# Kernel optimization log

Hardware: AMD Instinct MI355X
Metric: run time of the kernel (lower is better)

## Reference

```python
import jax, jax.numpy as jnp
import numpy as np

B, T, C = 64, 4096, 256
H = 4
HD = C // H  # head_dim = 64
EPS = 1e-5   # torch LayerNorm default


def setup_inputs() -> dict:
    key = jax.random.key(0)
    ks = jax.random.split(key, 8)
    x = jax.random.normal(ks[0], (B, T, C), dtype=jnp.float32)
    # per-head score MLP: Linear(C->HD) + Tanh + Linear(HD->1, no bias)
    W1 = jax.random.normal(ks[1], (H, C, HD), dtype=jnp.float32) * (1.0 / np.sqrt(C))
    b1 = jax.random.normal(ks[2], (H, HD), dtype=jnp.float32) * 0.02
    w2 = jax.random.normal(ks[3], (H, HD), dtype=jnp.float32) * (1.0 / np.sqrt(HD))
    # output projection Linear(H*C -> C), torch layout (out, in)
    Wo = jax.random.normal(ks[4], (C, H * C), dtype=jnp.float32) * (1.0 / np.sqrt(H * C))
    bo = jax.random.normal(ks[5], (C,), dtype=jnp.float32) * 0.02
    gamma = jnp.ones((C,), dtype=jnp.float32)
    beta = jnp.zeros((C,), dtype=jnp.float32)
    return {"x": x, "W1": W1, "b1": b1, "w2": w2, "Wo": Wo, "bo": bo,
            "gamma": gamma, "beta": beta}


def reference(x, W1, b1, w2, Wo, bo, gamma, beta):
    # All heads batched: hidden (B,H,T,HD)
    h = jnp.tanh(jnp.einsum('btc,hcd->bhtd', x, W1) + b1[None, :, None, :])
    scores = jnp.einsum('bhtd,hd->bht', h, w2)            # (B,H,T)
    weights = jax.nn.softmax(scores, axis=-1)             # softmax over T
    contexts = jnp.einsum('bht,btc->bhc', weights, x)     # (B,H,C)
    multi = contexts.reshape(B, H * C)                    # concat over heads
    out = multi @ Wo.T + bo                               # Linear(H*C->C)
    # LayerNorm over last dim (dropout is identity in eval mode)
    mu = jnp.mean(out, axis=-1, keepdims=True)
    var = jnp.mean(jnp.square(out - mu), axis=-1, keepdims=True)
    out = (out - mu) * jax.lax.rsqrt(var + EPS) * gamma + beta
    return out, weights
```

## Files before the change

kernel.cpp:

```cpp
#include <hip/hip_runtime.h>
#include <hip/hip_bf16.h>
#include <math.h>

#define B_ 64
#define T_ 4096
#define C_ 256
#define H_ 4
#define HD_ 64
#define EPS_ 1e-5f

#define TILE_ 64
#define NBLK_ 64

typedef __attribute__((ext_vector_type(4))) float floatx4;
typedef __attribute__((ext_vector_type(8))) short short8;

#if __has_builtin(__builtin_amdgcn_cvt_pk_bf16_f32)
typedef __attribute__((ext_vector_type(2))) __bf16 bf16x2_t;
__device__ __forceinline__ unsigned int pack_bf16x2(float a, float b) {
    bf16x2_t v = __builtin_amdgcn_cvt_pk_bf16_f32(a, b);
    return __builtin_bit_cast(unsigned int, v);
}
#else
__device__ __forceinline__ unsigned int pack_bf16x2(float a, float b) {
    unsigned int ua = __builtin_bit_cast(unsigned int, a);
    unsigned int ub = __builtin_bit_cast(unsigned int, b);
    ua = (ua + 0x7fffu + ((ua >> 16) & 1u)) >> 16;
    ub = (ub + 0x7fffu + ((ub >> 16) & 1u)) >> 16;
    return ua | (ub << 16);
}
#endif

__device__ __forceinline__ float fast_tanh(float v) {
    float t = v * 2.8853900817779268f;
#if __has_builtin(__builtin_amdgcn_exp2f)
    float e2 = __builtin_amdgcn_exp2f(t);
#else
    float e2 = exp2f(t);
#endif
#if __has_builtin(__builtin_amdgcn_rcpf)
    return fmaf(-2.0f, __builtin_amdgcn_rcpf(e2 + 1.0f), 1.0f);
#else
    return 1.0f - 2.0f / (e2 + 1.0f);
#endif
}

__global__ void k0_w1frag(const float* __restrict__ W1, uint4* __restrict__ w1f) {
    int h  = blockIdx.x >> 3;
    int ks = blockIdx.x & 7;
    int nb = threadIdx.x >> 6;
    int l  = threadIdx.x & 63;
    int nl = l & 15, q = l >> 4;
    int d  = nb * 16 + nl;
    const float* src = W1 + ((long)h * C_ + ks * 32 + q * 8) * HD_ + d;
    float v[8];
    #pragma unroll
    for (int j = 0; j < 8; ++j) v[j] = src[j * HD_];
    uint4 ua;
    ua.x = pack_bf16x2(v[0], v[1]); ua.y = pack_bf16x2(v[2], v[3]);
    ua.z = pack_bf16x2(v[4], v[5]); ua.w = pack_bf16x2(v[6], v[7]);
    w1f[((long)blockIdx.x * 4 + nb) * 64 + l] = ua;
}

#define ASTRIDE 264
__global__ __launch_bounds__(256, 4)
void k1_fused(const float* __restrict__ x, const uint4* __restrict__ w1f,
              const float* __restrict__ b1, const float* __restrict__ w2,
              float* __restrict__ rawscore, float* __restrict__ ctxp,
              float* __restrict__ mS) {
    __shared__ __align__(16) unsigned short shA[TILE_ * ASTRIDE];
    __shared__ float sS[4 * TILE_];
    __shared__ __align__(16) float sP4[TILE_ * 4];

    const int tid  = threadIdx.x;
    const int lane = tid & 63;
    const int w    = tid >> 6;
    const int nl   = lane & 15;
    const int q    = lane >> 4;
    const int rowbase = blockIdx.x * TILE_;
    const int b       = blockIdx.x >> 6;
    const int tbase   = (blockIdx.x & 63) * TILE_;

    const int arow = tid >> 2;
    const int acol = (tid & 3) * 8;
    const float* aptr = x + (long)(rowbase + arow) * C_ + acol;
    #pragma unroll
    for (int kc = 0; kc < 8; ++kc) {
        const float4* ap = (const float4*)(aptr + kc * 32);
        float4 f0 = ap[0], f1 = ap[1];
        uint4 ua;
        ua.x = pack_bf16x2(f0.x, f0.y); ua.y = pack_bf16x2(f0.z, f0.w);
        ua.z = pack_bf16x2(f1.x, f1.y); ua.w = pack_bf16x2(f1.z, f1.w);
        *(uint4*)&shA[arow * ASTRIDE + kc * 32 + acol] = ua;
    }

    floatx4 acc[4][4];
    #pragma unroll
    for (int i = 0; i < 4; ++i)
        #pragma unroll
        for (int j = 0; j < 4; ++j)
            acc[i][j] = (floatx4){0.f, 0.f, 0.f, 0.f};

    const uint4* bW = w1f + (long)w * (8 * 4 * 64) + lane;

    uint4 bFa[4], bFb[4];
    #pragma unroll
    for (int nb = 0; nb < 4; ++nb) bFa[nb] = bW[nb * 64];

    __syncthreads();

    #pragma unroll
    for (int kp = 0; kp < 4; ++kp) {
        const int ks0 = 2 * kp, ks1 = 2 * kp + 1;
        #pragma unroll
        for (int nb = 0; nb < 4; ++nb) bFb[nb] = bW[(ks1 * 4 + nb) * 64];
        #pragma unroll
        for (int mb = 0; mb < 4; ++mb) {
            short8 a = *(const short8*)&shA[(mb * 16 + nl) * ASTRIDE + ks0 * 32 + q * 8];
            #pragma unroll
            for (int nb = 0; nb < 4; ++nb)
                acc[mb][nb] = __builtin_amdgcn_mfma_f32_16x16x32_bf16(
                    a, __builtin_bit_cast(short8, bFa[nb]), acc[mb][nb], 0, 0, 0);
        }
        if (kp < 3) {
            #pragma unroll
            for (int nb = 0; nb < 4; ++nb) bFa[nb] = bW[((ks0 + 2) * 4 + nb) * 64];
        }
        #pragma unroll
        for (int mb = 0; mb < 4; ++mb) {
            short8 a = *(const short8*)&shA[(mb * 16 + nl) * ASTRIDE + ks1 * 32 + q * 8];
            #pragma unroll
            for (int nb = 0; nb < 4; ++nb)
                acc[mb][nb] = __builtin_amdgcn_mfma_f32_16x16x32_bf16(
                    a, __builtin_bit_cast(short8, bFb[nb]), acc[mb][nb], 0, 0, 0);
        }
    }

    float b1v[4], w2v[4];
    #pragma unroll
    for (int nb = 0; nb < 4; ++nb) {
        int d = nb * 16 + nl;
        b1v[nb] = b1[w * HD_ + d];
        w2v[nb] = w2[w * HD_ + d];
    }
    #pragma unroll
    for (int mb = 0; mb < 4; ++mb) {
        float p[4];
        #pragma unroll
        for (int r = 0; r < 4; ++r) {
            float s = 0.f;
            #pragma unroll
            for (int nb = 0; nb < 4; ++nb)
                s += fast_tanh(acc[mb][nb][r] + b1v[nb]) * w2v[nb];
            p[r] = s;
        }
        #pragma unroll
        for (int m = 1; m < 16; m <<= 1)
            #pragma unroll
            for (int r = 0; r < 4; ++r)
                p[r] += __shfl_xor(p[r], m, 64);
        if (nl == 0) {
            #pragma unroll
            for (int r = 0; r < 4; ++r)
                sS[w * TILE_ + mb * 16 + q * 4 + r] = p[r];
        }
    }

    {
        float s = sS[w * TILE_ + lane];
        float m = s;
        #pragma unroll
        for (int off = 1; off < 64; off <<= 1)
            m = fmaxf(m, __shfl_xor(m, off, 64));
        float e = __expf(s - m);
        float Ss = e;
        #pragma unroll
        for (int off = 1; off < 64; off <<= 1)
            Ss += __shfl_xor(Ss, off, 64);
        sP4[lane * 4 + w] = e;
        rawscore[((long)(b * H_ + w)) * T_ + tbase + lane] = s;
        if (lane == 0) {
            mS[((long)blockIdx.x * H_ + w) * 2 + 0] = m;
            mS[((long)blockIdx.x * H_ + w) * 2 + 1] = Ss;
        }
    }
    __syncthreads();

    {
        float c0 = 0.f, c1 = 0.f, c2 = 0.f, c3 = 0.f;
        const float* xr = x + (long)rowbase * C_ + tid;
        const float4* pv4 = (const float4*)sP4;
        #pragma unroll 8
        for (int t = 0; t < TILE_; ++t) {
            float xv = xr[(long)t * C_];
            float4 pv = pv4[t];
            c0 += pv.x * xv;
            c1 += pv.y * xv;
            c2 += pv.z * xv;
            c3 += pv.w * xv;
        }
        float* o = ctxp + (long)blockIdx.x * (H_ * C_) + tid;
        o[0]   = c0;
        o[256] = c1;
        o[512] = c2;
        o[768] = c3;
    }
}

__global__ __launch_bounds__(1024)
void k2_combine(const float* __restrict__ ctxp, const float* __restrict__ mS,
                float* __restrict__ gms, float* __restrict__ multi) {
    __shared__ float sm[NBLK_], sSl[NBLK_];
    __shared__ float red[4][256];
    int bh = blockIdx.x;
    int b = bh >> 2, h = bh & 3;
    int tid = threadIdx.x;
    int c  = tid & 255;
    int js = tid >> 8;
    if (tid < NBLK_) {
        long blk = (long)b * NBLK_ + tid;
        sm[tid]  = mS[(blk * H_ + h) * 2 + 0];
        sSl[tid] = mS[(blk * H_ + h) * 2 + 1];
    }
    __syncthreads();
    float m = -INFINITY;
    #pragma unroll 8
    for (int j = 0; j < NBLK_; ++j) m = fmaxf(m, sm[j]);
    float S = 0.f;
    #pragma unroll 8
    for (int j = 0; j < NBLK_; ++j) S += sSl[j] * __expf(sm[j] - m);
    float invS = 1.0f / S;
    if (tid == 0) { gms[bh * 2 + 0] = m; gms[bh * 2 + 1] = invS; }

    float acc = 0.f;
    #pragma unroll
    for (int jj = 0; jj < NBLK_ / 4; ++jj) {
        int j = js * (NBLK_ / 4) + jj;
        acc += ctxp[((long)(b * NBLK_ + j) * H_ + h) * C_ + c] * __expf(sm[j] - m);
    }
    red[js][c] = acc;
    __syncthreads();
    if (js == 0)
        multi[(long)b * (H_ * C_) + h * C_ + c] =
            (red[0][c] + red[1][c] + red[2][c] + red[3][c]) * invS;
}

__global__ void k3_weights(const float* __restrict__ gms, float* __restrict__ weights) {
    int bh = blockIdx.x >> 1, half = blockIdx.x & 1;
    float m = gms[bh * 2 + 0], invS = gms[bh * 2 + 1];
    float4* wr = (float4*)(weights + (long)bh * T_ + half * 2048);
    int tid = threadIdx.x;
    #pragma unroll
    for (int i = 0; i < 2; ++i) {
        float4 v = wr[tid + i * 256];
        v.x = __expf(v.x - m) * invS;
        v.y = __expf(v.y - m) * invS;
        v.z = __expf(v.z - m) * invS;
        v.w = __expf(v.w - m) * invS;
        wr[tid + i * 256] = v;
    }
}

__global__ __launch_bounds__(256)
void k4a_proj(const float* __restrict__ multiG, const float* __restrict__ Wo,
              const float* __restrict__ bo, float* __restrict__ outraw) {
    __shared__ __align__(16) float multi[1024];
    int b = blockIdx.x >> 4, cs = blockIdx.x & 15;
    int tid = threadIdx.x, w = tid >> 6, l = tid & 63;
    ((float4*)multi)[tid] = ((const float4*)(multiG + (long)b * 1024))[tid];
    __syncthreads();
    float a[4];
    #pragma unroll
    for (int cc = 0; cc < 4; ++cc) {
        int c = cs * 16 + w * 4 + cc;
        const float4* wrow = (const float4*)(Wo + (long)c * 1024);
        const float4* mv = (const float4*)multi;
        float s = 0.f;
        #pragma unroll
        for (int k = 0; k < 4; ++k) {
            float4 wv = wrow[k * 64 + l];
            float4 m4 = mv[k * 64 + l];
            s += wv.x * m4.x + wv.y * m4.y + wv.z * m4.z + wv.w * m4.w;
        }
        a[cc] = s;
    }
    #pragma unroll
    for (int off = 1; off < 64; off <<= 1)
        #pragma unroll
        for (int cc = 0; cc < 4; ++cc)
            a[cc] += __shfl_xor(a[cc], off, 64);
    if (l == 0) {
        #pragma unroll
        for (int cc = 0; cc < 4; ++cc) {
            int c = cs * 16 + w * 4 + cc;
            outraw[(long)b * C_ + c] = a[cc] + bo[c];
        }
    }
}

__global__ void k4b_ln(const float* __restrict__ outraw, const float* __restrict__ gamma,
                       const float* __restrict__ beta, float* __restrict__ out) {
    __shared__ float red[256];
    int b = blockIdx.x, tid = threadIdx.x;
    float acc = outraw[(long)b * C_ + tid];
    red[tid] = acc; __syncthreads();
    for (int st = 128; st > 0; st >>= 1) {
        if (tid < st) red[tid] += red[tid + st];
        __syncthreads();
    }
    float mu = red[0] * (1.0f / 256.0f); __syncthreads();
    float dv = acc - mu;
    red[tid] = dv * dv; __syncthreads();
    for (int st = 128; st > 0; st >>= 1) {
        if (tid < st) red[tid] += red[tid + st];
        __syncthreads();
    }
    float var = red[0] * (1.0f / 256.0f);
    out[(long)b * C_ + tid] = dv * rsqrtf(var + EPS_) * gamma[tid] + beta[tid];
}

extern "C" void kernel_launch(void* const* d_in, const int* in_sizes, int n_in,
                              void* d_out, int out_size, void* d_ws, size_t ws_size,
                              hipStream_t stream) {
    const float* x     = (const float*)d_in[0];
    const float* W1    = (const float*)d_in[1];
    const float* b1    = (const float*)d_in[2];
    const float* w2    = (const float*)d_in[3];
    const float* Wo    = (const float*)d_in[4];
    const float* bo    = (const float*)d_in[5];
    const float* gamma = (const float*)d_in[6];
    const float* beta  = (const float*)d_in[7];

    float* out     = (float*)d_out;
    float* weights = out + B_ * C_;

    const long NB = (long)B_ * NBLK_;
    float* ctxp   = (float*)d_ws;
    float* mS     = ctxp + NB * (H_ * C_);
    float* multi  = mS + NB * H_ * 2;
    uint4* w1f    = (uint4*)(multi + B_ * H_ * C_);
    float* gms    = (float*)w1f + 32768;
    float* outraw = gms + 512;

    k0_w1frag <<<32, 256, 0, stream>>>(W1, w1f);
    k1_fused  <<<NB, 256, 0, stream>>>(x, w1f, b1, w2, weights, ctxp, mS);
    k2_combine<<<256, 1024, 0, stream>>>(ctxp, mS, gms, multi);
    k3_weights<<<512, 256, 0, stream>>>(gms, weights);
    k4a_proj  <<<1024, 256, 0, stream>>>(multi, Wo, bo, outraw);
    k4b_ln    <<<64, 256, 0, stream>>>(outraw, gamma, beta, out);
}
```

Baseline: 423.5 us.

## Make k1 persistent over four tiles with prefetch of the next x tile

k1_fused now launches 1024 blocks, and each block walks four consecutive 64-row tiles instead of one tile per block. While the scoring and softmax of the current tile run, the block loads the next x tile from global memory, converts it to bf16 and writes it into shared memory. The shared-memory write is split into two halves around a barrier so it does not overwrite data still being read. This is meant to hide global load latency and cut per-block launch overhead, at the cost of higher register pressure, fewer blocks in flight, and an extra barrier per tile.

```diff
diff --git a/kernel.cpp b/kernel.cpp
--- a/kernel.cpp
+++ b/kernel.cpp
@@ -11,6 +11,8 @@
 
 #define TILE_ 64
 #define NBLK_ 64
+#define NT_ 4
+#define GRID1_ 1024
 
 typedef __attribute__((ext_vector_type(4))) float floatx4;
 typedef __attribute__((ext_vector_type(8))) short short8;
@@ -77,64 +79,10 @@
     const int w    = tid >> 6;
     const int nl   = lane & 15;
     const int q    = lane >> 4;
-    const int rowbase = blockIdx.x * TILE_;
-    const int b       = blockIdx.x >> 6;
-    const int tbase   = (blockIdx.x & 63) * TILE_;
-
     const int arow = tid >> 2;
     const int acol = (tid & 3) * 8;
-    const float* aptr = x + (long)(rowbase + arow) * C_ + acol;
-    #pragma unroll
-    for (int kc = 0; kc < 8; ++kc) {
-        const float4* ap = (const float4*)(aptr + kc * 32);
-        float4 f0 = ap[0], f1 = ap[1];
-        uint4 ua;
-        ua.x = pack_bf16x2(f0.x, f0.y); ua.y = pack_bf16x2(f0.z, f0.w);
-        ua.z = pack_bf16x2(f1.x, f1.y); ua.w = pack_bf16x2(f1.z, f1.w);
-        *(uint4*)&shA[arow * ASTRIDE + kc * 32 + acol] = ua;
-    }
-
-    floatx4 acc[4][4];
-    #pragma unroll
-    for (int i = 0; i < 4; ++i)
-        #pragma unroll
-        for (int j = 0; j < 4; ++j)
-            acc[i][j] = (floatx4){0.f, 0.f, 0.f, 0.f};
 
     const uint4* bW = w1f + (long)w * (8 * 4 * 64) + lane;
-
-    uint4 bFa[4], bFb[4];
-    #pragma unroll
-    for (int nb = 0; nb < 4; ++nb) bFa[nb] = bW[nb * 64];
-
-    __syncthreads();
-
-    #pragma unroll
-    for (int kp = 0; kp < 4; ++kp) {
-        const int ks0 = 2 * kp, ks1 = 2 * kp + 1;
-        #pragma unroll
-        for (int nb = 0; nb < 4; ++nb) bFb[nb] = bW[(ks1 * 4 + nb) * 64];
-        #pragma unroll
-        for (int mb = 0; mb < 4; ++mb) {
-            short8 a = *(const short8*)&shA[(mb * 16 + nl) * ASTRIDE + ks0 * 32 + q * 8];
-            #pragma unroll
-            for (int nb = 0; nb < 4; ++nb)
-                acc[mb][nb] = __builtin_amdgcn_mfma_f32_16x16x32_bf16(
-                    a, __builtin_bit_cast(short8, bFa[nb]), acc[mb][nb], 0, 0, 0);
-        }
-        if (kp < 3) {
-            #pragma unroll
-            for (int nb = 0; nb < 4; ++nb) bFa[nb] = bW[((ks0 + 2) * 4 + nb) * 64];
-        }
-        #pragma unroll
-        for (int mb = 0; mb < 4; ++mb) {
-            short8 a = *(const short8*)&shA[(mb * 16 + nl) * ASTRIDE + ks1 * 32 + q * 8];
-            #pragma unroll
-            for (int nb = 0; nb < 4; ++nb)
-                acc[mb][nb] = __builtin_amdgcn_mfma_f32_16x16x32_bf16(
-                    a, __builtin_bit_cast(short8, bFb[nb]), acc[mb][nb], 0, 0, 0);
-        }
-    }
 
     float b1v[4], w2v[4];
     #pragma unroll
@@ -143,67 +91,180 @@
         b1v[nb] = b1[w * HD_ + d];
         w2v[nb] = w2[w * HD_ + d];
     }
-    #pragma unroll
-    for (int mb = 0; mb < 4; ++mb) {
-        float p[4];
-        #pragma unroll
-        for (int r = 0; r < 4; ++r) {
-            float s = 0.f;
-            #pragma unroll
-            for (int nb = 0; nb < 4; ++nb)
-                s += fast_tanh(acc[mb][nb][r] + b1v[nb]) * w2v[nb];
-            p[r] = s;
-        }
-        #pragma unroll
-        for (int m = 1; m < 16; m <<= 1)
-            #pragma unroll
-            for (int r = 0; r < 4; ++r)
-                p[r] += __shfl_xor(p[r], m, 64);
-        if (nl == 0) {
-            #pragma unroll
-            for (int r = 0; r < 4; ++r)
-                sS[w * TILE_ + mb * 16 + q * 4 + r] = p[r];
-        }
-    }
 
     {
-        float s = sS[w * TILE_ + lane];
-        float m = s;
-        #pragma unroll
-        for (int off = 1; off < 64; off <<= 1)
-            m = fmaxf(m, __shfl_xor(m, off, 64));
-        float e = __expf(s - m);
-        float Ss = e;
-        #pragma unroll
-        for (int off = 1; off < 64; off <<= 1)
-            Ss += __shfl_xor(Ss, off, 64);
-        sP4[lane * 4 + w] = e;
-        rawscore[((long)(b * H_ + w)) * T_ + tbase + lane] = s;
-        if (lane == 0) {
-            mS[((long)blockIdx.x * H_ + w) * 2 + 0] = m;
-            mS[((long)blockIdx.x * H_ + w) * 2 + 1] = Ss;
-        }
-    }
+        const int rb0 = (blockIdx.x * NT_) * TILE_;
+        const float* aptr = x + (long)(rb0 + arow) * C_ + acol;
+        #pragma unroll
+        for (int kc = 0; kc < 8; ++kc) {
+            const float4* ap = (const float4*)(aptr + kc * 32);
+            float4 f0 = ap[0], f1 = ap[1];
+            uint4 ua;
+            ua.x = pack_bf16x2(f0.x, f0.y); ua.y = pack_bf16x2(f0.z, f0.w);
+            ua.z = pack_bf16x2(f1.x, f1.y); ua.w = pack_bf16x2(f1.z, f1.w);
+            *(uint4*)&shA[arow * ASTRIDE + kc * 32 + acol] = ua;
+        }
+    }
+    uint4 bFa[4], bFb[4];
+    #pragma unroll
+    for (int nb = 0; nb < 4; ++nb) bFa[nb] = bW[nb * 64];
     __syncthreads();
 
-    {
-        float c0 = 0.f, c1 = 0.f, c2 = 0.f, c3 = 0.f;
-        const float* xr = x + (long)rowbase * C_ + tid;
-        const float4* pv4 = (const float4*)sP4;
-        #pragma unroll 8
-        for (int t = 0; t < TILE_; ++t) {
-            float xv = xr[(long)t * C_];
-            float4 pv = pv4[t];
-            c0 += pv.x * xv;
-            c1 += pv.y * xv;
-            c2 += pv.z * xv;
-            c3 += pv.w * xv;
-        }
-        float* o = ctxp + (long)blockIdx.x * (H_ * C_) + tid;
-        o[0]   = c0;
-        o[256] = c1;
-        o[512] = c2;
-        o[768] = c3;
+    #pragma unroll 1
+    for (int it = 0; it < NT_; ++it) {
+        const int tile    = blockIdx.x * NT_ + it;
+        const int rowbase = tile * TILE_;
+        const int b       = tile >> 6;
+        const int tbase   = (tile & 63) * TILE_;
+        const bool more   = (it + 1 < NT_);
+        const float* aN   = x + (long)(rowbase + TILE_ + arow) * C_ + acol;
+
+        floatx4 acc[4][4];
+        #pragma unroll
+        for (int i = 0; i < 4; ++i)
+            #pragma unroll
+            for (int j = 0; j < 4; ++j)
+                acc[i][j] = (floatx4){0.f, 0.f, 0.f, 0.f};
+        #pragma unroll
+        for (int kp = 0; kp < 4; ++kp) {
+            const int ks0 = 2 * kp, ks1 = 2 * kp + 1;
+            #pragma unroll
+            for (int nb = 0; nb < 4; ++nb) bFb[nb] = bW[(ks1 * 4 + nb) * 64];
+            #pragma unroll
+            for (int mb = 0; mb < 4; ++mb) {
+                short8 a = *(const short8*)&shA[(mb * 16 + nl) * ASTRIDE + ks0 * 32 + q * 8];
+                #pragma unroll
+                for (int nb = 0; nb < 4; ++nb)
+                    acc[mb][nb] = __builtin_amdgcn_mfma_f32_16x16x32_bf16(
+                        a, __builtin_bit_cast(short8, bFa[nb]), acc[mb][nb], 0, 0, 0);
+            }
+            if (kp < 3) {
+                #pragma unroll
+                for (int nb = 0; nb < 4; ++nb) bFa[nb] = bW[((ks0 + 2) * 4 + nb) * 64];
+            }
+            #pragma unroll
+            for (int mb = 0; mb < 4; ++mb) {
+                short8 a = *(const short8*)&shA[(mb * 16 + nl) * ASTRIDE + ks1 * 32 + q * 8];
+                #pragma unroll
+                for (int nb = 0; nb < 4; ++nb)
+                    acc[mb][nb] = __builtin_amdgcn_mfma_f32_16x16x32_bf16(
+                        a, __builtin_bit_cast(short8, bFb[nb]), acc[mb][nb], 0, 0, 0);
+            }
+        }
+        #pragma unroll
+        for (int nb = 0; nb < 4; ++nb) bFa[nb] = bW[nb * 64];
+
+        float4 f0h[4], f1h[4];
+        if (more) {
+            #pragma unroll
+            for (int kc = 0; kc < 4; ++kc) {
+                const float4* ap = (const float4*)(aN + kc * 32);
+                f0h[kc] = ap[0]; f1h[kc] = ap[1];
+            }
+        }
+
+        #pragma unroll
+        for (int mb = 0; mb < 4; ++mb) {
+            float p[4];
+            #pragma unroll
+            for (int r = 0; r < 4; ++r) {
+                float s = 0.f;
+                #pragma unroll
+                for (int nb = 0; nb < 4; ++nb)
+                    s += fast_tanh(acc[mb][nb][r] + b1v[nb]) * w2v[nb];
+                p[r] = s;
+            }
+            #pragma unroll
+            for (int m = 1; m < 16; m <<= 1)
+                #pragma unroll
+                for (int r = 0; r < 4; ++r)
+                    p[r] += __shfl_xor(p[r], m, 64);
+            if (nl == 0) {
+                #pragma unroll
+                for (int r = 0; r < 4; ++r)
+                    sS[w * TILE_ + mb * 16 + q * 4 + r] = p[r];
+            }
+        }
+
+        uint4 stA[4];
+        if (more) {
+            #pragma unroll
+            for (int kc = 0; kc < 4; ++kc) {
+                stA[kc].x = pack_bf16x2(f0h[kc].x, f0h[kc].y);
+                stA[kc].y = pack_bf16x2(f0h[kc].z, f0h[kc].w);
+                stA[kc].z = pack_bf16x2(f1h[kc].x, f1h[kc].y);
+                stA[kc].w = pack_bf16x2(f1h[kc].z, f1h[kc].w);
+            }
+        }
+
+        {
+            float s = sS[w * TILE_ + lane];
+            float m = s;
+            #pragma unroll
+            for (int off = 1; off < 64; off <<= 1)
+                m = fmaxf(m, __shfl_xor(m, off, 64));
+            float e = __expf(s - m);
+            float Ss = e;
+            #pragma unroll
+            for (int off = 1; off < 64; off <<= 1)
+                Ss += __shfl_xor(Ss, off, 64);
+            sP4[lane * 4 + w] = e;
+            rawscore[((long)(b * H_ + w)) * T_ + tbase + lane] = s;
+            if (lane == 0) {
+                mS[((long)tile * H_ + w) * 2 + 0] = m;
+                mS[((long)tile * H_ + w) * 2 + 1] = Ss;
+            }
+        }
+
+        float4 f0g[4], f1g[4];
+        if (more) {
+            #pragma unroll
+            for (int kc = 0; kc < 4; ++kc) {
+                const float4* ap = (const float4*)(aN + (kc + 4) * 32);
+                f0g[kc] = ap[0]; f1g[kc] = ap[1];
+            }
+        }
+
+        __syncthreads();
+
+        if (more) {
+            #pragma unroll
+            for (int kc = 0; kc < 4; ++kc)
+                *(uint4*)&shA[arow * ASTRIDE + kc * 32 + acol] = stA[kc];
+        }
+
+        {
+            float c0 = 0.f, c1 = 0.f, c2 = 0.f, c3 = 0.f;
+            const float* xr = x + (long)rowbase * C_ + tid;
+            const float4* pv4 = (const float4*)sP4;
+            #pragma unroll 8
+            for (int t = 0; t < TILE_; ++t) {
+                float xv = xr[(long)t * C_];
+                float4 pv = pv4[t];
+                c0 += pv.x * xv;
+                c1 += pv.y * xv;
+                c2 += pv.z * xv;
+                c3 += pv.w * xv;
+            }
+            float* o = ctxp + (long)tile * (H_ * C_) + tid;
+            o[0]   = c0;
+            o[256] = c1;
+            o[512] = c2;
+            o[768] = c3;
+        }
+
+        if (more) {
+            #pragma unroll
+            for (int kc = 0; kc < 4; ++kc) {
+                uint4 ub;
+                ub.x = pack_bf16x2(f0g[kc].x, f0g[kc].y);
+                ub.y = pack_bf16x2(f0g[kc].z, f0g[kc].w);
+                ub.z = pack_bf16x2(f1g[kc].x, f1g[kc].y);
+                ub.w = pack_bf16x2(f1g[kc].z, f1g[kc].w);
+                *(uint4*)&shA[arow * ASTRIDE + (kc + 4) * 32 + acol] = ub;
+            }
+            __syncthreads();
+        }
     }
 }
 
@@ -343,7 +404,7 @@
     float* outraw = gms + 512;
 
     k0_w1frag <<<32, 256, 0, stream>>>(W1, w1f);
-    k1_fused  <<<NB, 256, 0, stream>>>(x, w1f, b1, w2, weights, ctxp, mS);
+    k1_fused  <<<GRID1_, 256, 0, stream>>>(x, w1f, b1, w2, weights, ctxp, mS);
     k2_combine<<<256, 1024, 0, stream>>>(ctxp, mS, gms, multi);
     k3_weights<<<512, 256, 0, stream>>>(gms, weights);
     k4a_proj  <<<1024, 256, 0, stream>>>(multi, Wo, bo, outraw);
```

New measurement: 734.5 us. +73.4%, slower.

## Fold softmax normalization into combine kernel and fuse projection with LayerNorm

Applied to the files above, without the earlier changes.

The separate weights-normalization kernel is removed: the combine kernel now rescales each (b,h) row of raw scores (1024 threads × float4 = 4096) with the global max and inverse sum it has just computed. The output projection and LayerNorm are merged into one 64-block kernel of 1024 threads that keeps the projected row in shared memory. This cuts two kernel launches and the intermediate buffers for max/sum and the raw projection output. The trade-off is that the fused projection runs on only 64 blocks instead of 1024, so each block streams the full Wo matrix with less parallelism.

```diff
diff --git a/kernel.cpp b/kernel.cpp
--- a/kernel.cpp
+++ b/kernel.cpp
@@ -209,7 +209,7 @@
 
 __global__ __launch_bounds__(1024)
 void k2_combine(const float* __restrict__ ctxp, const float* __restrict__ mS,
-                float* __restrict__ gms, float* __restrict__ multi) {
+                float* __restrict__ weights, float* __restrict__ multi) {
     __shared__ float sm[NBLK_], sSl[NBLK_];
     __shared__ float red[4][256];
     int bh = blockIdx.x;
@@ -230,93 +230,79 @@
     #pragma unroll 8
     for (int j = 0; j < NBLK_; ++j) S += sSl[j] * __expf(sm[j] - m);
     float invS = 1.0f / S;
-    if (tid == 0) { gms[bh * 2 + 0] = m; gms[bh * 2 + 1] = invS; }
-
-    float acc = 0.f;
-    #pragma unroll
-    for (int jj = 0; jj < NBLK_ / 4; ++jj) {
-        int j = js * (NBLK_ / 4) + jj;
-        acc += ctxp[((long)(b * NBLK_ + j) * H_ + h) * C_ + c] * __expf(sm[j] - m);
-    }
-    red[js][c] = acc;
-    __syncthreads();
-    if (js == 0)
-        multi[(long)b * (H_ * C_) + h * C_ + c] =
-            (red[0][c] + red[1][c] + red[2][c] + red[3][c]) * invS;
-}
-
-__global__ void k3_weights(const float* __restrict__ gms, float* __restrict__ weights) {
-    int bh = blockIdx.x >> 1, half = blockIdx.x & 1;
-    float m = gms[bh * 2 + 0], invS = gms[bh * 2 + 1];
-    float4* wr = (float4*)(weights + (long)bh * T_ + half * 2048);
-    int tid = threadIdx.x;
-    #pragma unroll
-    for (int i = 0; i < 2; ++i) {
-        float4 v = wr[tid + i * 256];
+
+    {
+        float4* wr = (float4*)(weights + (long)bh * T_);
+        float4 v = wr[tid];
         v.x = __expf(v.x - m) * invS;
         v.y = __expf(v.y - m) * invS;
         v.z = __expf(v.z - m) * invS;
         v.w = __expf(v.w - m) * invS;
-        wr[tid + i * 256] = v;
-    }
-}
-
-__global__ __launch_bounds__(256)
-void k4a_proj(const float* __restrict__ multiG, const float* __restrict__ Wo,
-              const float* __restrict__ bo, float* __restrict__ outraw) {
-    __shared__ __align__(16) float multi[1024];
-    int b = blockIdx.x >> 4, cs = blockIdx.x & 15;
-    int tid = threadIdx.x, w = tid >> 6, l = tid & 63;
-    ((float4*)multi)[tid] = ((const float4*)(multiG + (long)b * 1024))[tid];
-    __syncthreads();
-    float a[4];
-    #pragma unroll
-    for (int cc = 0; cc < 4; ++cc) {
-        int c = cs * 16 + w * 4 + cc;
+        wr[tid] = v;
+    }
+
+    float acc = 0.f;
+    #pragma unroll
+    for (int jj = 0; jj < NBLK_ / 4; ++jj) {
+        int j = js * (NBLK_ / 4) + jj;
+        acc += ctxp[((long)(b * NBLK_ + j) * H_ + h) * C_ + c] * __expf(sm[j] - m);
+    }
+    red[js][c] = acc;
+    __syncthreads();
+    if (js == 0)
+        multi[(long)b * (H_ * C_) + h * C_ + c] =
+            (red[0][c] + red[1][c] + red[2][c] + red[3][c]) * invS;
+}
+
+__global__ __launch_bounds__(1024)
+void k4_fused(const float* __restrict__ multiG, const float* __restrict__ Wo,
+              const float* __restrict__ bo, const float* __restrict__ gamma,
+              const float* __restrict__ beta, float* __restrict__ out) {
+    __shared__ float sOut[256];
+    __shared__ float red[256];
+    int b = blockIdx.x, tid = threadIdx.x, w = tid >> 6, l = tid & 63;
+
+    float4 mreg[4];
+    const float4* mv = (const float4*)(multiG + (long)b * 1024);
+    #pragma unroll
+    for (int k = 0; k < 4; ++k) mreg[k] = mv[k * 64 + l];
+
+    #pragma unroll
+    for (int cc = 0; cc < 16; ++cc) {
+        int c = w * 16 + cc;
         const float4* wrow = (const float4*)(Wo + (long)c * 1024);
-        const float4* mv = (const float4*)multi;
         float s = 0.f;
         #pragma unroll
         for (int k = 0; k < 4; ++k) {
             float4 wv = wrow[k * 64 + l];
-            float4 m4 = mv[k * 64 + l];
-            s += wv.x * m4.x + wv.y * m4.y + wv.z * m4.z + wv.w * m4.w;
-        }
-        a[cc] = s;
-    }
-    #pragma unroll
-    for (int off = 1; off < 64; off <<= 1)
-        #pragma unroll
-        for (int cc = 0; cc < 4; ++cc)
-            a[cc] += __shfl_xor(a[cc], off, 64);
-    if (l == 0) {
-        #pragma unroll
-        for (int cc = 0; cc < 4; ++cc) {
-            int c = cs * 16 + w * 4 + cc;
-            outraw[(long)b * C_ + c] = a[cc] + bo[c];
-        }
-    }
-}
-
-__global__ void k4b_ln(const float* __restrict__ outraw, const float* __restrict__ gamma,
-                       const float* __restrict__ beta, float* __restrict__ out) {
-    __shared__ float red[256];
-    int b = blockIdx.x, tid = threadIdx.x;
-    float acc = outraw[(long)b * C_ + tid];
-    red[tid] = acc; __syncthreads();
+            s += wv.x * mreg[k].x + wv.y * mreg[k].y + wv.z * mreg[k].z + wv.w * mreg[k].w;
+        }
+        #pragma unroll
+        for (int off = 1; off < 64; off <<= 1)
+            s += __shfl_xor(s, off, 64);
+        if (l == 0) sOut[c] = s + bo[c];
+    }
+    __syncthreads();
+
+    float acc = 0.f;
+    if (tid < 256) { acc = sOut[tid]; red[tid] = acc; }
+    __syncthreads();
     for (int st = 128; st > 0; st >>= 1) {
         if (tid < st) red[tid] += red[tid + st];
         __syncthreads();
     }
-    float mu = red[0] * (1.0f / 256.0f); __syncthreads();
+    float mu = red[0] * (1.0f / 256.0f);
+    __syncthreads();
     float dv = acc - mu;
-    red[tid] = dv * dv; __syncthreads();
+    if (tid < 256) red[tid] = dv * dv;
+    __syncthreads();
     for (int st = 128; st > 0; st >>= 1) {
         if (tid < st) red[tid] += red[tid + st];
         __syncthreads();
     }
     float var = red[0] * (1.0f / 256.0f);
-    out[(long)b * C_ + tid] = dv * rsqrtf(var + EPS_) * gamma[tid] + beta[tid];
+    if (tid < 256)
+        out[(long)b * C_ + tid] = dv * rsqrtf(var + EPS_) * gamma[tid] + beta[tid];
 }
 
 extern "C" void kernel_launch(void* const* d_in, const int* in_sizes, int n_in,
@@ -339,13 +325,9 @@
     float* mS     = ctxp + NB * (H_ * C_);
     float* multi  = mS + NB * H_ * 2;
     uint4* w1f    = (uint4*)(multi + B_ * H_ * C_);
-    float* gms    = (float*)w1f + 32768;
-    float* outraw = gms + 512;
 
     k0_w1frag <<<32, 256, 0, stream>>>(W1, w1f);
     k1_fused  <<<NB, 256, 0, stream>>>(x, w1f, b1, w2, weights, ctxp, mS);
-    k2_combine<<<256, 1024, 0, stream>>>(ctxp, mS, gms, multi);
-    k3_weights<<<512, 256, 0, stream>>>(gms, weights);
-    k4a_proj  <<<1024, 256, 0, stream>>>(multi, Wo, bo, outraw);
-    k4b_ln    <<<64, 256, 0, stream>>>(outraw, gamma, beta, out);
-}
+    k2_combine<<<256, 1024, 0, stream>>>(ctxp, mS, weights, multi);
+    k4_fused  <<<64, 1024, 0, stream>>>(multi, Wo, bo, gamma, beta, out);
+}
```

Result: slower. 433.7 us (+2.4%).
